# Kernel optimization log

Measured on AMD Instinct MI355X. Metric: run time of the kernel, lower is better.

## Reference

```python
import jax, jax.numpy as jnp
import numpy as np

NH = 8  # n heads
HD = 64  # head dim (dim // nhead)


def setup_inputs() -> dict:
    key = jax.random.key(0)
    ks = jax.random.split(key, 6)
    bs, T, nj, dim = 8, 256, 24, 512
    # xavier_uniform over last two dims of [nj, dim, dim]: bound = sqrt(6/(dim+dim))
    bound = float(np.sqrt(6.0 / (dim + dim)))
    x = jax.random.normal(ks[0], (bs, T, nj, dim), dtype=jnp.float32)
    Wq = jax.random.uniform(ks[1], (nj, dim, dim), minval=-bound, maxval=bound, dtype=jnp.float32)
    Wk = jax.random.uniform(ks[2], (nj, dim, dim), minval=-bound, maxval=bound, dtype=jnp.float32)
    Wv = jax.random.uniform(ks[3], (nj, dim, dim), minval=-bound, maxval=bound, dtype=jnp.float32)
    lb = float(np.sqrt(1.0 / dim))  # nn.Linear default init bound
    Wo = jax.random.uniform(ks[4], (dim, dim), minval=-lb, maxval=lb, dtype=jnp.float32)
    bo = jax.random.uniform(ks[5], (dim,), minval=-lb, maxval=lb, dtype=jnp.float32)
    return {"x": x, "Wq": Wq, "Wk": Wk, "Wv": Wv, "Wo": Wo, "bo": bo}


def reference(x, Wq, Wk, Wv, Wo, bo):
    bs, T, nj, dim = x.shape
    nh, hd = NH, HD
    # per-joint grouped projections: btjd,jde->btje
    q = jnp.einsum('btjd,jde->btje', x, Wq)
    k = jnp.einsum('btjd,jde->btje', x, Wk)
    v = jnp.einsum('btjd,jde->btje', x, Wv)
    # split heads and move time to attention axis: (bs, nj, nh, T, hd)
    def split(t):
        return t.reshape(bs, T, nj, nh, hd).transpose(0, 2, 3, 1, 4)
    q, k, v = split(q), split(k), split(v)
    scores = jnp.einsum('bjhtd,bjhsd->bjhts', q, k) * (hd ** -0.5)
    attn = jax.nn.softmax(scores, axis=-1)  # dropout is identity in eval mode
    out = jnp.einsum('bjhts,bjhsd->bjhtd', attn, v)
    out = out.transpose(0, 3, 1, 2, 4).reshape(bs, T, nj, dim)
    # torch Linear: y = x @ W^T + b
    return jnp.einsum('btjd,ed->btje', out, Wo) + bo
```

## Files before the change

kernel.cpp:

```cpp
#include <hip/hip_runtime.h>

typedef _Float16 f16;
typedef _Float16 f16x8 __attribute__((ext_vector_type(8)));
typedef _Float16 f16x4 __attribute__((ext_vector_type(4)));
typedef float    f32x4 __attribute__((ext_vector_type(4)));

constexpr int kBS  = 8;
constexpr int kT   = 256;
constexpr int kNJ  = 24;
constexpr int kDIM = 512;
constexpr int kNH  = 8;
constexpr int kHD  = 64;
constexpr int kRS  = kNJ * kDIM;
constexpr int kBT  = kBS * kT;
constexpr int kROWS = kBT * kNJ;

__device__ __forceinline__ void gload_lds16(const void* g, void* l) {
  auto gp = (const __attribute__((address_space(1))) unsigned int*)g;
  auto lp = (__attribute__((address_space(3))) unsigned int*)l;
  __builtin_amdgcn_global_load_lds(gp, lp, 16, 0, 0);
}

__global__ __launch_bounds__(256) void k_cvt(const float* __restrict__ in,
                                             f16* __restrict__ out, int n4) {
  int i = blockIdx.x * blockDim.x + threadIdx.x;
  int stride = gridDim.x * blockDim.x;
  for (; i < n4; i += stride) {
    float4 v = ((const float4*)in)[i];
    f16x4 h;
    h[0] = (f16)v.x; h[1] = (f16)v.y; h[2] = (f16)v.z; h[3] = (f16)v.w;
    ((f16x4*)out)[i] = h;
  }
}

__global__ __launch_bounds__(256) void k_cvt_wT(const float* __restrict__ W,
                                                f16* __restrict__ WT) {
  int bx = blockIdx.x;
  int et = bx & 15, dt = bx >> 4;
  int j  = blockIdx.y;
  __shared__ float tile[32][33];
  int tid = threadIdx.x;
  int r = tid >> 3, c4 = (tid & 7) * 4;
  const float* src = W + ((size_t)j * 512 + (dt * 32 + r)) * 512 + et * 32 + c4;
  float4 v = *(const float4*)src;
  tile[r][c4 + 0] = v.x; tile[r][c4 + 1] = v.y;
  tile[r][c4 + 2] = v.z; tile[r][c4 + 3] = v.w;
  __syncthreads();
  f16x4 h;
  h[0] = (f16)tile[c4 + 0][r]; h[1] = (f16)tile[c4 + 1][r];
  h[2] = (f16)tile[c4 + 2][r]; h[3] = (f16)tile[c4 + 3][r];
  f16* dst = WT + ((size_t)j * 512 + (et * 32 + r)) * 512 + dt * 32 + c4;
  *(f16x4*)dst = h;
}

template <bool OUT_F32>
__device__ __forceinline__ void gemm_tile_128(const f16* __restrict__ A, int lda,
                                              const f16* __restrict__ Bt,
                                              void* __restrict__ Cp, int ldc,
                                              const float* __restrict__ bias) {
  __shared__ f16 As[128 * 64];
  __shared__ f16 Bs[128 * 64];
  int tid = threadIdx.x, lane = tid & 63, wave = tid >> 6;
  int wm = wave >> 1, wn = wave & 1;
  int lr = lane >> 3, cs = lane & 7;
  int fr = lane & 15, fq = lane >> 4;
  f32x4 acc[4][4] = {};

  for (int k0 = 0; k0 < 512; k0 += 64) {
    for (int i = 0; i < 4; ++i) {
      int row = wave * 32 + i * 8 + lr;
      int csrc = cs ^ (row & 7);
      gload_lds16(A + (size_t)row * lda + k0 + csrc * 8, As + (wave * 32 + i * 8) * 64);
      gload_lds16(Bt + (size_t)row * 512 + k0 + csrc * 8, Bs + (wave * 32 + i * 8) * 64);
    }
    __syncthreads();
    for (int kc = 0; kc < 2; ++kc) {
      f16x8 af[4], bf[4];
      for (int m = 0; m < 4; ++m) {
        int row = wm * 64 + m * 16 + fr;
        int chunk = kc * 4 + fq;
        af[m] = *(const f16x8*)((const char*)As + row * 128 + ((chunk ^ (row & 7)) << 4));
      }
      for (int n = 0; n < 4; ++n) {
        int row = wn * 64 + n * 16 + fr;
        int chunk = kc * 4 + fq;
        bf[n] = *(const f16x8*)((const char*)Bs + row * 128 + ((chunk ^ (row & 7)) << 4));
      }
      for (int m = 0; m < 4; ++m)
        for (int n = 0; n < 4; ++n)
          acc[m][n] = __builtin_amdgcn_mfma_f32_16x16x32_f16(af[m], bf[n], acc[m][n], 0, 0, 0);
    }
    __syncthreads();
  }
  for (int m = 0; m < 4; ++m)
    for (int n = 0; n < 4; ++n)
      for (int r = 0; r < 4; ++r) {
        int row = wm * 64 + m * 16 + fq * 4 + r;
        int col = wn * 64 + n * 16 + fr;
        if constexpr (OUT_F32) {
          ((float*)Cp)[(size_t)row * ldc + col] = acc[m][n][r] + bias[col];
        } else {
          ((f16*)Cp)[(size_t)row * ldc + col] = (f16)acc[m][n][r];
        }
      }
}

__global__ __launch_bounds__(256) void k_qkv(const f16* __restrict__ xh,
                                             const f16* __restrict__ wT,
                                             f16* __restrict__ q, f16* __restrict__ k,
                                             f16* __restrict__ v) {
  int bid = blockIdx.x;
  int nt = bid & 3, mt = bid >> 2;
  int j = blockIdx.y, sel = blockIdx.z;
  const f16* A = xh + (size_t)j * kDIM + (size_t)mt * 128 * kRS;
  const f16* Bt = wT + ((size_t)sel * kNJ + j) * 262144 + (size_t)nt * 128 * 512;
  f16* outp = (sel == 0) ? q : (sel == 1) ? k : v;
  f16* C = outp + (size_t)j * kDIM + (size_t)mt * 128 * kRS + nt * 128;
  gemm_tile_128<false>(A, kRS, Bt, C, kRS, nullptr);
}

__global__ __launch_bounds__(256) void k_outproj(const f16* __restrict__ O,
                                                 const f16* __restrict__ woh,
                                                 const float* __restrict__ bo,
                                                 float* __restrict__ y) {
  int bid = blockIdx.x;
  int nt = bid & 3, mt = bid >> 2;
  const f16* A = O + (size_t)mt * 128 * 512;
  const f16* Bt = woh + (size_t)nt * 128 * 512;
  float* C = y + (size_t)mt * 128 * 512 + nt * 128;
  gemm_tile_128<true>(A, 512, Bt, C, 512, bo + nt * 128);
}

__global__ __launch_bounds__(256) void k_attn(const f16* __restrict__ q,
                                              const f16* __restrict__ k,
                                              const f16* __restrict__ v,
                                              f16* __restrict__ o) {
  int bid = blockIdx.x;
  int h = bid & 7, j = (bid >> 3) % kNJ, b = bid / (kNH * kNJ);
  __shared__ f16 Ks[256 * 64];
  __shared__ f16 Vt[64 * 256];
  __shared__ f16 Ps[4 * 16 * 256];
  int tid = threadIdx.x, lane = tid & 63, wave = tid >> 6;
  int fr = lane & 15, fq = lane >> 4;
  size_t base = ((size_t)b * kT * kNJ + j) * kDIM + h * kHD;

  for (int i = 0; i < 8; ++i) {
    int row = wave * 64 + i * 8 + (lane >> 3);
    int csrc = (lane & 7) ^ (row & 7);
    gload_lds16(k + base + (size_t)row * kRS + csrc * 8, Ks + (wave * 64 + i * 8) * 64);
  }
  for (int i = 0; i < 8; ++i) {
    int s = i * 32 + (tid >> 3);
    int d0 = (tid & 7) * 8;
    f16x8 vv = *(const f16x8*)(v + base + (size_t)s * kRS + d0);
    for (int u = 0; u < 8; ++u) {
      int d = d0 + u;
      int chunk = s >> 3;
      int byteoff = d * 512 + (((chunk ^ (d & 7))) << 4) + (s & 7) * 2;
      *(f16*)((char*)Vt + byteoff) = vv[u];
    }
  }
  __syncthreads();

  f16* P = Ps + wave * 16 * 256;
  for (int qt = 0; qt < 4; ++qt) {
    int trow = wave * 64 + qt * 16 + fr;
    const f16* qrow = q + base + (size_t)trow * kRS + fq * 8;
    f16x8 qa0 = *(const f16x8*)(qrow);
    f16x8 qa1 = *(const f16x8*)(qrow + 32);

    f32x4 s_acc[16] = {};
    for (int ct = 0; ct < 16; ++ct) {
      {
        int row = ct * 16 + fr, chunk = fq;
        f16x8 bf = *(const f16x8*)((const char*)Ks + row * 128 + ((chunk ^ (row & 7)) << 4));
        s_acc[ct] = __builtin_amdgcn_mfma_f32_16x16x32_f16(qa0, bf, s_acc[ct], 0, 0, 0);
      }
      {
        int row = ct * 16 + fr, chunk = 4 + fq;
        f16x8 bf = *(const f16x8*)((const char*)Ks + row * 128 + ((chunk ^ (row & 7)) << 4));
        s_acc[ct] = __builtin_amdgcn_mfma_f32_16x16x32_f16(qa1, bf, s_acc[ct], 0, 0, 0);
      }
    }

    const float scale = 0.125f;
    float linv[4];
    for (int r = 0; r < 4; ++r) {
      float m = -1e30f;
      for (int ct = 0; ct < 16; ++ct) m = fmaxf(m, s_acc[ct][r]);
      for (int dd = 1; dd < 16; dd <<= 1) m = fmaxf(m, __shfl_xor(m, dd));
      m *= scale;
      float lsum = 0.f;
      for (int ct = 0; ct < 16; ++ct) {
        float p = __expf(s_acc[ct][r] * scale - m);
        s_acc[ct][r] = p;
        lsum += p;
      }
      for (int dd = 1; dd < 16; dd <<= 1) lsum += __shfl_xor(lsum, dd);
      linv[r] = 1.0f / lsum;
    }

    for (int ct = 0; ct < 16; ++ct)
      for (int r = 0; r < 4; ++r) {
        int row = fq * 4 + r;
        int col = ct * 16 + fr;
        int chunk = col >> 3;
        int byteoff = row * 512 + ((chunk ^ (row & 7)) << 4) + (col & 7) * 2;
        *(f16*)((char*)P + byteoff) = (f16)s_acc[ct][r];
      }

    f16x8 pa[8];
    for (int kc = 0; kc < 8; ++kc) {
      int row = fr, chunk = kc * 4 + fq;
      pa[kc] = *(const f16x8*)((const char*)P + row * 512 + ((chunk ^ (row & 7)) << 4));
    }
    f32x4 oacc[4] = {};
    for (int nt = 0; nt < 4; ++nt)
      for (int kc = 0; kc < 8; ++kc) {
        int row = nt * 16 + fr, chunk = kc * 4 + fq;
        f16x8 bf = *(const f16x8*)((const char*)Vt + row * 512 + ((chunk ^ (row & 7)) << 4));
        oacc[nt] = __builtin_amdgcn_mfma_f32_16x16x32_f16(pa[kc], bf, oacc[nt], 0, 0, 0);
      }

    for (int r = 0; r < 4; ++r) {
      int trow2 = wave * 64 + qt * 16 + fq * 4 + r;
      for (int nt = 0; nt < 4; ++nt) {
        int d = nt * 16 + fr;
        o[base + (size_t)trow2 * kRS + d] = (f16)(oacc[nt][r] * linv[r]);
      }
    }
  }
}

extern "C" void kernel_launch(void* const* d_in, const int* in_sizes, int n_in,
                              void* d_out, int out_size, void* d_ws, size_t ws_size,
                              hipStream_t stream) {
  const float* x  = (const float*)d_in[0];
  const float* Wq = (const float*)d_in[1];
  const float* Wk = (const float*)d_in[2];
  const float* Wv = (const float*)d_in[3];
  const float* Wo = (const float*)d_in[4];
  const float* bo = (const float*)d_in[5];
  float* y = (float*)d_out;

  char* ws = (char*)d_ws;
  f16* xh  = (f16*)(ws);
  f16* wT  = (f16*)(ws + 50331648);
  f16* woh = (f16*)(ws + 88080384);
  f16* q   = (f16*)(ws + 88604672);
  f16* k   = (f16*)(ws + 138936320);
  f16* v   = (f16*)(ws + 189267968);
  f16* o   = xh;

  k_cvt<<<4096, 256, 0, stream>>>(x, xh, (kBS * kT * kNJ * kDIM) / 4);
  k_cvt<<<256, 256, 0, stream>>>(Wo, woh, (kDIM * kDIM) / 4);
  dim3 gT(256, kNJ);
  k_cvt_wT<<<gT, 256, 0, stream>>>(Wq, wT);
  k_cvt_wT<<<gT, 256, 0, stream>>>(Wk, wT + 6291456);
  k_cvt_wT<<<gT, 256, 0, stream>>>(Wv, wT + 12582912);

  k_qkv<<<dim3(64, kNJ, 3), 256, 0, stream>>>(xh, wT, q, k, v);
  k_attn<<<kBS * kNJ * kNH, 256, 0, stream>>>(q, k, v, o);
  k_outproj<<<1536, 256, 0, stream>>>(o, woh, bo, y);
}
```

Before: 569.8 us.

## Reorganize QKV layouts to head-major, transpose V in projection, keep P in registers

The x conversion now writes a joint-major f16 copy so each projection GEMM reads contiguous rows. Q and K are stored head-contiguous and V is stored pre-transposed, which lets attention load K and V^T straight into LDS with async loads instead of strided gathers and scalar scatter stores. Attention computes S transposed (K as the A operand), so the softmax probabilities stay in registers and feed a 16x16x16 MFMA directly, removing the P round trip through LDS. It also remaps block order in the QKV GEMM and adds unroll pragmas and a two-blocks-per-CU launch bound. The cost is more complex indexing and narrower MFMA instructions in the PV step.

```diff
diff --git a/kernel.cpp b/kernel.cpp
--- a/kernel.cpp
+++ b/kernel.cpp
@@ -13,12 +13,29 @@
 constexpr int kHD  = 64;
 constexpr int kRS  = kNJ * kDIM;
 constexpr int kBT  = kBS * kT;
-constexpr int kROWS = kBT * kNJ;
+constexpr int kHEADSZ = kT * kHD;
 
 __device__ __forceinline__ void gload_lds16(const void* g, void* l) {
   auto gp = (const __attribute__((address_space(1))) unsigned int*)g;
   auto lp = (__attribute__((address_space(3))) unsigned int*)l;
   __builtin_amdgcn_global_load_lds(gp, lp, 16, 0, 0);
+}
+
+__global__ __launch_bounds__(256) void k_cvt_xj(const float* __restrict__ in,
+                                                f16* __restrict__ out, int n4) {
+  int i = blockIdx.x * blockDim.x + threadIdx.x;
+  int stride = gridDim.x * blockDim.x;
+  for (; i < n4; i += stride) {
+    float4 v = ((const float4*)in)[i];
+    f16x4 h;
+    h[0] = (f16)v.x; h[1] = (f16)v.y; h[2] = (f16)v.z; h[3] = (f16)v.w;
+    int e0 = i * 4;
+    int R = e0 / kRS;
+    int rem = e0 - R * kRS;
+    int j = rem >> 9;
+    int d = rem & 511;
+    ((f16x4*)out)[j * 262144 + R * 128 + (d >> 2)] = h;
+  }
 }
 
 __global__ __launch_bounds__(256) void k_cvt(const float* __restrict__ in,
@@ -53,181 +70,224 @@
   *(f16x4*)dst = h;
 }
 
-template <bool OUT_F32>
-__device__ __forceinline__ void gemm_tile_128(const f16* __restrict__ A, int lda,
-                                              const f16* __restrict__ Bt,
-                                              void* __restrict__ Cp, int ldc,
-                                              const float* __restrict__ bias) {
-  __shared__ f16 As[128 * 64];
-  __shared__ f16 Bs[128 * 64];
+__device__ __forceinline__ void gemm_acc_128(const f16* __restrict__ A,
+                                             const f16* __restrict__ Bt,
+                                             f32x4 (&acc)[4][4],
+                                             f16* As, f16* Bs) {
   int tid = threadIdx.x, lane = tid & 63, wave = tid >> 6;
   int wm = wave >> 1, wn = wave & 1;
   int lr = lane >> 3, cs = lane & 7;
   int fr = lane & 15, fq = lane >> 4;
-  f32x4 acc[4][4] = {};
 
   for (int k0 = 0; k0 < 512; k0 += 64) {
+#pragma unroll
     for (int i = 0; i < 4; ++i) {
       int row = wave * 32 + i * 8 + lr;
       int csrc = cs ^ (row & 7);
-      gload_lds16(A + (size_t)row * lda + k0 + csrc * 8, As + (wave * 32 + i * 8) * 64);
+      gload_lds16(A + (size_t)row * 512 + k0 + csrc * 8, As + (wave * 32 + i * 8) * 64);
       gload_lds16(Bt + (size_t)row * 512 + k0 + csrc * 8, Bs + (wave * 32 + i * 8) * 64);
     }
     __syncthreads();
+#pragma unroll
     for (int kc = 0; kc < 2; ++kc) {
       f16x8 af[4], bf[4];
+#pragma unroll
       for (int m = 0; m < 4; ++m) {
         int row = wm * 64 + m * 16 + fr;
         int chunk = kc * 4 + fq;
         af[m] = *(const f16x8*)((const char*)As + row * 128 + ((chunk ^ (row & 7)) << 4));
       }
+#pragma unroll
       for (int n = 0; n < 4; ++n) {
         int row = wn * 64 + n * 16 + fr;
         int chunk = kc * 4 + fq;
         bf[n] = *(const f16x8*)((const char*)Bs + row * 128 + ((chunk ^ (row & 7)) << 4));
       }
+#pragma unroll
       for (int m = 0; m < 4; ++m)
+#pragma unroll
         for (int n = 0; n < 4; ++n)
           acc[m][n] = __builtin_amdgcn_mfma_f32_16x16x32_f16(af[m], bf[n], acc[m][n], 0, 0, 0);
     }
     __syncthreads();
   }
-  for (int m = 0; m < 4; ++m)
-    for (int n = 0; n < 4; ++n)
-      for (int r = 0; r < 4; ++r) {
-        int row = wm * 64 + m * 16 + fq * 4 + r;
-        int col = wn * 64 + n * 16 + fr;
-        if constexpr (OUT_F32) {
-          ((float*)Cp)[(size_t)row * ldc + col] = acc[m][n][r] + bias[col];
-        } else {
-          ((f16*)Cp)[(size_t)row * ldc + col] = (f16)acc[m][n][r];
-        }
-      }
 }
 
 __global__ __launch_bounds__(256) void k_qkv(const f16* __restrict__ xh,
                                              const f16* __restrict__ wT,
                                              f16* __restrict__ q, f16* __restrict__ k,
                                              f16* __restrict__ v) {
+  __shared__ f16 As[128 * 64];
+  __shared__ f16 Bs[128 * 64];
   int bid = blockIdx.x;
-  int nt = bid & 3, mt = bid >> 2;
+  int s = (bid & 7) * 8 + (bid >> 3);
+  int nt = s & 3, mt = s >> 2;
   int j = blockIdx.y, sel = blockIdx.z;
-  const f16* A = xh + (size_t)j * kDIM + (size_t)mt * 128 * kRS;
+  const f16* A = xh + (size_t)j * 1048576 + (size_t)mt * 128 * 512;
   const f16* Bt = wT + ((size_t)sel * kNJ + j) * 262144 + (size_t)nt * 128 * 512;
-  f16* outp = (sel == 0) ? q : (sel == 1) ? k : v;
-  f16* C = outp + (size_t)j * kDIM + (size_t)mt * 128 * kRS + nt * 128;
-  gemm_tile_128<false>(A, kRS, Bt, C, kRS, nullptr);
+  f32x4 acc[4][4] = {};
+  gemm_acc_128(A, Bt, acc, As, Bs);
+
+  int lane = threadIdx.x & 63, wave = threadIdx.x >> 6;
+  int wm = wave >> 1, wn = wave & 1;
+  int fr = lane & 15, fq = lane >> 4;
+  if (sel < 2) {
+    f16* dst = (sel == 0) ? q : k;
+#pragma unroll
+    for (int m = 0; m < 4; ++m)
+#pragma unroll
+      for (int n = 0; n < 4; ++n) {
+        int colb = nt * 128 + wn * 64 + n * 16;
+        int h = colb >> 6, d0 = colb & 63;
+        int R0 = mt * 128 + wm * 64 + m * 16 + fq * 4;
+        int b = R0 >> 8, t0 = R0 & 255;
+        size_t hb = ((size_t)(b * kNJ + j) * kNH + h) * kHEADSZ;
+#pragma unroll
+        for (int r = 0; r < 4; ++r)
+          dst[hb + (size_t)(t0 + r) * 64 + d0 + fr] = (f16)acc[m][n][r];
+      }
+  } else {
+#pragma unroll
+    for (int m = 0; m < 4; ++m)
+#pragma unroll
+      for (int n = 0; n < 4; ++n) {
+        int colb = nt * 128 + wn * 64 + n * 16;
+        int h = colb >> 6, d0 = colb & 63;
+        int R0 = mt * 128 + wm * 64 + m * 16 + fq * 4;
+        int b = R0 >> 8, t0 = R0 & 255;
+        size_t hb = ((size_t)(b * kNJ + j) * kNH + h) * kHEADSZ;
+        f16x4 ov;
+#pragma unroll
+        for (int r = 0; r < 4; ++r) ov[r] = (f16)acc[m][n][r];
+        *(f16x4*)(v + hb + (size_t)(d0 + fr) * kT + t0) = ov;
+      }
+  }
 }
 
 __global__ __launch_bounds__(256) void k_outproj(const f16* __restrict__ O,
                                                  const f16* __restrict__ woh,
                                                  const float* __restrict__ bo,
                                                  float* __restrict__ y) {
+  __shared__ f16 As[128 * 64];
+  __shared__ f16 Bs[128 * 64];
   int bid = blockIdx.x;
   int nt = bid & 3, mt = bid >> 2;
   const f16* A = O + (size_t)mt * 128 * 512;
   const f16* Bt = woh + (size_t)nt * 128 * 512;
   float* C = y + (size_t)mt * 128 * 512 + nt * 128;
-  gemm_tile_128<true>(A, 512, Bt, C, 512, bo + nt * 128);
-}
-
-__global__ __launch_bounds__(256) void k_attn(const f16* __restrict__ q,
-                                              const f16* __restrict__ k,
-                                              const f16* __restrict__ v,
-                                              f16* __restrict__ o) {
+  f32x4 acc[4][4] = {};
+  gemm_acc_128(A, Bt, acc, As, Bs);
+
+  int lane = threadIdx.x & 63, wave = threadIdx.x >> 6;
+  int wm = wave >> 1, wn = wave & 1;
+  int fr = lane & 15, fq = lane >> 4;
+  const float* bias = bo + nt * 128;
+#pragma unroll
+  for (int m = 0; m < 4; ++m)
+#pragma unroll
+    for (int n = 0; n < 4; ++n)
+#pragma unroll
+      for (int r = 0; r < 4; ++r) {
+        int row = wm * 64 + m * 16 + fq * 4 + r;
+        int col = wn * 64 + n * 16 + fr;
+        C[(size_t)row * 512 + col] = acc[m][n][r] + bias[col];
+      }
+}
+
+__global__ __launch_bounds__(256, 2) void k_attn(const f16* __restrict__ q,
+                                                 const f16* __restrict__ k,
+                                                 const f16* __restrict__ v,
+                                                 f16* __restrict__ o) {
   int bid = blockIdx.x;
   int h = bid & 7, j = (bid >> 3) % kNJ, b = bid / (kNH * kNJ);
   __shared__ f16 Ks[256 * 64];
   __shared__ f16 Vt[64 * 256];
-  __shared__ f16 Ps[4 * 16 * 256];
   int tid = threadIdx.x, lane = tid & 63, wave = tid >> 6;
   int fr = lane & 15, fq = lane >> 4;
-  size_t base = ((size_t)b * kT * kNJ + j) * kDIM + h * kHD;
-
+  size_t hb = ((size_t)(b * kNJ + j) * kNH + h) * kHEADSZ;
+  const f16* qh = q + hb;
+  const f16* kh = k + hb;
+  const f16* vth = v + hb;
+
+#pragma unroll
   for (int i = 0; i < 8; ++i) {
     int row = wave * 64 + i * 8 + (lane >> 3);
-    int csrc = (lane & 7) ^ (row & 7);
-    gload_lds16(k + base + (size_t)row * kRS + csrc * 8, Ks + (wave * 64 + i * 8) * 64);
-  }
-  for (int i = 0; i < 8; ++i) {
-    int s = i * 32 + (tid >> 3);
-    int d0 = (tid & 7) * 8;
-    f16x8 vv = *(const f16x8*)(v + base + (size_t)s * kRS + d0);
-    for (int u = 0; u < 8; ++u) {
-      int d = d0 + u;
-      int chunk = s >> 3;
-      int byteoff = d * 512 + (((chunk ^ (d & 7))) << 4) + (s & 7) * 2;
-      *(f16*)((char*)Vt + byteoff) = vv[u];
-    }
+    int g = (lane & 7) ^ (row & 7);
+    gload_lds16(kh + row * 64 + g * 8, Ks + (wave * 64 + i * 8) * 64);
+  }
+#pragma unroll
+  for (int p = 0; p < 8; ++p) {
+    int off = wave * 8192 + p * 1024 + lane * 16;
+    int d = off >> 9;
+    int cs = (off >> 4) & 31;
+    int g = cs ^ (d & 7);
+    gload_lds16(vth + d * 256 + g * 8, (char*)Vt + wave * 8192 + p * 1024);
   }
   __syncthreads();
 
-  f16* P = Ps + wave * 16 * 256;
+  const float scale = 0.125f;
   for (int qt = 0; qt < 4; ++qt) {
     int trow = wave * 64 + qt * 16 + fr;
-    const f16* qrow = q + base + (size_t)trow * kRS + fq * 8;
+    const f16* qrow = qh + trow * 64 + fq * 8;
     f16x8 qa0 = *(const f16x8*)(qrow);
     f16x8 qa1 = *(const f16x8*)(qrow + 32);
 
     f32x4 s_acc[16] = {};
+#pragma unroll
     for (int ct = 0; ct < 16; ++ct) {
-      {
-        int row = ct * 16 + fr, chunk = fq;
-        f16x8 bf = *(const f16x8*)((const char*)Ks + row * 128 + ((chunk ^ (row & 7)) << 4));
-        s_acc[ct] = __builtin_amdgcn_mfma_f32_16x16x32_f16(qa0, bf, s_acc[ct], 0, 0, 0);
-      }
-      {
-        int row = ct * 16 + fr, chunk = 4 + fq;
-        f16x8 bf = *(const f16x8*)((const char*)Ks + row * 128 + ((chunk ^ (row & 7)) << 4));
-        s_acc[ct] = __builtin_amdgcn_mfma_f32_16x16x32_f16(qa1, bf, s_acc[ct], 0, 0, 0);
-      }
-    }
-
-    const float scale = 0.125f;
-    float linv[4];
-    for (int r = 0; r < 4; ++r) {
-      float m = -1e30f;
-      for (int ct = 0; ct < 16; ++ct) m = fmaxf(m, s_acc[ct][r]);
-      for (int dd = 1; dd < 16; dd <<= 1) m = fmaxf(m, __shfl_xor(m, dd));
-      m *= scale;
-      float lsum = 0.f;
-      for (int ct = 0; ct < 16; ++ct) {
-        float p = __expf(s_acc[ct][r] * scale - m);
+      int row = ct * 16 + fr;
+      f16x8 a0 = *(const f16x8*)((const char*)Ks + row * 128 + ((fq ^ (row & 7)) << 4));
+      s_acc[ct] = __builtin_amdgcn_mfma_f32_16x16x32_f16(a0, qa0, s_acc[ct], 0, 0, 0);
+      f16x8 a1 = *(const f16x8*)((const char*)Ks + row * 128 + (((4 + fq) ^ (row & 7)) << 4));
+      s_acc[ct] = __builtin_amdgcn_mfma_f32_16x16x32_f16(a1, qa1, s_acc[ct], 0, 0, 0);
+    }
+
+    float mx = -1e30f;
+#pragma unroll
+    for (int ct = 0; ct < 16; ++ct)
+#pragma unroll
+      for (int r = 0; r < 4; ++r) mx = fmaxf(mx, s_acc[ct][r]);
+    mx = fmaxf(mx, __shfl_xor(mx, 16));
+    mx = fmaxf(mx, __shfl_xor(mx, 32));
+    mx *= scale;
+    float lsum = 0.f;
+#pragma unroll
+    for (int ct = 0; ct < 16; ++ct)
+#pragma unroll
+      for (int r = 0; r < 4; ++r) {
+        float p = __expf(s_acc[ct][r] * scale - mx);
         s_acc[ct][r] = p;
         lsum += p;
       }
-      for (int dd = 1; dd < 16; dd <<= 1) lsum += __shfl_xor(lsum, dd);
-      linv[r] = 1.0f / lsum;
-    }
-
+    lsum += __shfl_xor(lsum, 16);
+    lsum += __shfl_xor(lsum, 32);
+    float linv = 1.0f / lsum;
+
+    f16x4 pb[16];
+#pragma unroll
     for (int ct = 0; ct < 16; ++ct)
-      for (int r = 0; r < 4; ++r) {
-        int row = fq * 4 + r;
-        int col = ct * 16 + fr;
-        int chunk = col >> 3;
-        int byteoff = row * 512 + ((chunk ^ (row & 7)) << 4) + (col & 7) * 2;
-        *(f16*)((char*)P + byteoff) = (f16)s_acc[ct][r];
-      }
-
-    f16x8 pa[8];
-    for (int kc = 0; kc < 8; ++kc) {
-      int row = fr, chunk = kc * 4 + fq;
-      pa[kc] = *(const f16x8*)((const char*)P + row * 512 + ((chunk ^ (row & 7)) << 4));
-    }
+#pragma unroll
+      for (int r = 0; r < 4; ++r) pb[ct][r] = (f16)s_acc[ct][r];
+
     f32x4 oacc[4] = {};
-    for (int nt = 0; nt < 4; ++nt)
-      for (int kc = 0; kc < 8; ++kc) {
-        int row = nt * 16 + fr, chunk = kc * 4 + fq;
-        f16x8 bf = *(const f16x8*)((const char*)Vt + row * 512 + ((chunk ^ (row & 7)) << 4));
-        oacc[nt] = __builtin_amdgcn_mfma_f32_16x16x32_f16(pa[kc], bf, oacc[nt], 0, 0, 0);
-      }
-
-    for (int r = 0; r < 4; ++r) {
-      int trow2 = wave * 64 + qt * 16 + fq * 4 + r;
-      for (int nt = 0; nt < 4; ++nt) {
-        int d = nt * 16 + fr;
-        o[base + (size_t)trow2 * kRS + d] = (f16)(oacc[nt][r] * linv[r]);
-      }
+#pragma unroll
+    for (int nt = 0; nt < 4; ++nt) {
+      int d = nt * 16 + fr;
+#pragma unroll
+      for (int ks = 0; ks < 16; ++ks) {
+        int byteoff = d * 512 + (((2 * ks + (fq >> 1)) ^ (d & 7)) << 4) + (fq & 1) * 8;
+        f16x4 va = *(const f16x4*)((const char*)Vt + byteoff);
+        oacc[nt] = __builtin_amdgcn_mfma_f32_16x16x16f16(va, pb[ks], oacc[nt], 0, 0, 0);
+      }
+    }
+
+    size_t ob = ((size_t)(b * kT + trow) * kNJ + j) * kDIM + h * kHD;
+#pragma unroll
+    for (int nt = 0; nt < 4; ++nt) {
+      f16x4 ov;
+#pragma unroll
+      for (int r = 0; r < 4; ++r) ov[r] = (f16)(oacc[nt][r] * linv);
+      *(f16x4*)(o + ob + nt * 16 + fq * 4) = ov;
     }
   }
 }
@@ -252,7 +312,7 @@
   f16* v   = (f16*)(ws + 189267968);
   f16* o   = xh;
 
-  k_cvt<<<4096, 256, 0, stream>>>(x, xh, (kBS * kT * kNJ * kDIM) / 4);
+  k_cvt_xj<<<4096, 256, 0, stream>>>(x, xh, (kBT * kRS) / 4);
   k_cvt<<<256, 256, 0, stream>>>(Wo, woh, (kDIM * kDIM) / 4);
   dim3 gT(256, kNJ);
   k_cvt_wT<<<gT, 256, 0, stream>>>(Wq, wT);
```

Measured after the change: 564.5 us. No clear change (-0.9%).
